# Kernel tuning notes

Hardware: AMD Instinct MI355X
Metric: run time of the kernel (lower is better)

## Reference

```python
import jax, jax.numpy as jnp
import numpy as np

B, N_TOK, C = 64, 256, 1024
H = 16
PH, PW = 16, 16  # patch (window) size; N_TOK == PH*PW
D_FF = 4 * C
EPS = 1e-5


def rel_pos_idx(ph, pw):
    # Swin-style relative position index for a ph x pw window -> [ph*pw * ph*pw]
    coords_h = np.arange(ph)
    coords_w = np.arange(pw)
    coords = np.stack(np.meshgrid(coords_h, coords_w, indexing='ij'))  # [2, ph, pw]
    coords = coords.reshape(2, -1)  # [2, N]
    rel = coords[:, :, None] - coords[:, None, :]  # [2, N, N]
    rel = rel.transpose(1, 2, 0)  # [N, N, 2]
    rel[:, :, 0] += ph - 1
    rel[:, :, 1] += pw - 1
    rel[:, :, 0] *= 2 * pw - 1
    return rel.sum(-1).reshape(-1).astype(np.int32)  # [N*N]


def layernorm(x, g, b):
    mu = jnp.mean(x, axis=-1, keepdims=True)
    var = jnp.mean(jnp.square(x - mu), axis=-1, keepdims=True)
    return (x - mu) * jax.lax.rsqrt(var + EPS) * g + b


def setup_inputs() -> dict:
    key = jax.random.key(0)
    ks = jax.random.split(key, 12)
    s = lambda fan: 1.0 / np.sqrt(fan)
    inp = {
        'x': jax.random.normal(ks[0], (B, N_TOK, C), dtype=jnp.float32),
        'rel_pos_idx': jnp.asarray(rel_pos_idx(PH, PW)),
        'qkv_w': jax.random.normal(ks[1], (C, 3 * C), dtype=jnp.float32) * s(C),
        'qkv_b': jnp.zeros((3 * C,), dtype=jnp.float32),
        'proj_w': jax.random.normal(ks[2], (C, C), dtype=jnp.float32) * s(C),
        'proj_b': jnp.zeros((C,), dtype=jnp.float32),
        'rel_pos_bias': jax.random.uniform(ks[3], ((2 * PH - 1) * (2 * PW - 1), H), dtype=jnp.float32),
        'ln1_g': jnp.ones((C,), dtype=jnp.float32),
        'ln1_b': jnp.zeros((C,), dtype=jnp.float32),
        'ln2_g': jnp.ones((C,), dtype=jnp.float32),
        'ln2_b': jnp.zeros((C,), dtype=jnp.float32),
        'fc1_w': jax.random.normal(ks[4], (C, D_FF), dtype=jnp.float32) * s(C),
        'fc1_b': jnp.zeros((D_FF,), dtype=jnp.float32),
        'fc2_w': jax.random.normal(ks[5], (D_FF, C), dtype=jnp.float32) * s(D_FF),
        'fc2_b': jnp.zeros((C,), dtype=jnp.float32),
    }
    return inp


def reference(x, rel_pos_idx, qkv_w, qkv_b, proj_w, proj_b, rel_pos_bias,
              ln1_g, ln1_b, ln2_g, ln2_b, fc1_w, fc1_b, fc2_w, fc2_b):
    Bc, N, Cc = x.shape
    Dh = Cc // H
    scale = Dh ** -0.5

    # --- token mixer: RelAttention with pre-norm residual ---
    h = layernorm(x, ln1_g, ln1_b)
    qkv = (h @ qkv_w + qkv_b).reshape(Bc, N, 3, H, Dh)
    qkv = jnp.transpose(qkv, (2, 0, 3, 1, 4))  # [3, B, H, N, Dh]
    q, k, v = qkv[0] * scale, qkv[1], qkv[2]

    attn = jnp.einsum('bhnd,bhmd->bhnm', q, k)  # [B, H, N, N]
    # gathered relative position bias: [N*N] -> [N, N, H] -> [H, N, N]
    bias = rel_pos_bias[rel_pos_idx].reshape(N, N, H)
    attn = attn + jnp.transpose(bias, (2, 0, 1))[None]
    attn = jax.nn.softmax(attn, axis=-1)

    out = jnp.einsum('bhnm,bhmd->bhnd', attn, v)  # [B, H, N, Dh]
    out = jnp.transpose(out, (0, 2, 1, 3)).reshape(Bc, N, Cc)  # MergeHeads
    x = x + (out @ proj_w + proj_b)

    # --- MLP with pre-norm residual ---
    h2 = layernorm(x, ln2_g, ln2_b)
    h2 = jax.nn.gelu(h2 @ fc1_w + fc1_b)
    x = x + (h2 @ fc2_w + fc2_b)
    return x
```

## Files before the change

kernel.cpp:

```cpp
#include <hip/hip_runtime.h>
#include <hip/hip_bf16.h>
#include <math.h>

typedef __hip_bfloat16 bf16;
typedef __attribute__((ext_vector_type(8))) __bf16 bf16x8;
typedef __attribute__((ext_vector_type(4))) float f32x4;
typedef __attribute__((ext_vector_type(4))) unsigned u32x4;

#define NB 64
#define NTOK 256
#define CDIM 1024
#define NH 16
#define DH 64
#define DFF 4096
#define MROWS (NB * NTOK)

__device__ __forceinline__ float gelu_f(float x) {
    float t = 1.5957691216057308f * (x + 0.044715f * x * x * x);
    return x / (1.0f + __expf(-t));
}

__device__ __forceinline__ void gload_lds16(const void* g, void* l) {
    __builtin_amdgcn_global_load_lds((const __attribute__((address_space(1))) void*)g,
                                     (__attribute__((address_space(3))) void*)l,
                                     16, 0, 0);
}

__global__ void transpose_f32_bf16(const float* __restrict__ in, bf16* __restrict__ out,
                                   int R, int Cc) {
    __shared__ bf16 tile[32][33];
    int c0 = blockIdx.x * 32, r0 = blockIdx.y * 32;
    int t = threadIdx.x;
    int r = t >> 5, c = t & 31;
#pragma unroll
    for (int i = 0; i < 4; i++)
        tile[r + i * 8][c] = (bf16)in[(size_t)(r0 + r + i * 8) * Cc + c0 + c];
    __syncthreads();
#pragma unroll
    for (int i = 0; i < 4; i++)
        out[(size_t)(c0 + r + i * 8) * R + r0 + c] = tile[c][r + i * 8];
}

__global__ __launch_bounds__(256) void ln_kernel(const float* __restrict__ xin,
                                                 const float* __restrict__ g,
                                                 const float* __restrict__ b,
                                                 bf16* __restrict__ outp) {
    __shared__ float red[8];
    int row = blockIdx.x, t = threadIdx.x;
    float4 v = ((const float4*)(xin + (size_t)row * CDIM))[t];
    float s = v.x + v.y + v.z + v.w;
    float q = v.x * v.x + v.y * v.y + v.z * v.z + v.w * v.w;
#pragma unroll
    for (int off = 32; off > 0; off >>= 1) {
        s += __shfl_down(s, off);
        q += __shfl_down(q, off);
    }
    int wave = t >> 6;
    if ((t & 63) == 0) { red[wave] = s; red[4 + wave] = q; }
    __syncthreads();
    float st = red[0] + red[1] + red[2] + red[3];
    float qt = red[4] + red[5] + red[6] + red[7];
    float mu = st * (1.0f / CDIM);
    float rstd = rsqrtf(qt * (1.0f / CDIM) - mu * mu + 1e-5f);
    float4 gv = ((const float4*)g)[t];
    float4 bv = ((const float4*)b)[t];
    bf16* orow = outp + (size_t)row * CDIM + t * 4;
    orow[0] = (bf16)((v.x - mu) * rstd * gv.x + bv.x);
    orow[1] = (bf16)((v.y - mu) * rstd * gv.y + bv.y);
    orow[2] = (bf16)((v.z - mu) * rstd * gv.z + bv.z);
    orow[3] = (bf16)((v.w - mu) * rstd * gv.w + bv.w);
}

__global__ void biasq_kernel(const int* __restrict__ idx, const float* __restrict__ rpb,
                             float* __restrict__ bq) {
    int e = blockIdx.x * 256 + threadIdx.x;
    int j = e & 3, lr = (e >> 2) & 15, ck = (e >> 6) & 3, q = (e >> 8) & 255, h = e >> 16;
    int k = ck * 64 + j * 16 + lr;
    bq[e] = rpb[idx[q * 256 + k] * NH + h];
}

__global__ __launch_bounds__(512, 2) void gemm_bt_kernel(
    const bf16* __restrict__ Abf, const bf16* __restrict__ Btbf,
    const float* __restrict__ bias, const float* resid,
    void* outp, size_t qstride, int M, int N, int K, int mode) {
    __shared__ __align__(16) u32x4 SL[4][2][1024];
    const unsigned short* A = (const unsigned short*)Abf;
    const unsigned short* Bt = (const unsigned short*)Btbf;
    int tid = threadIdx.x;
    int wave = tid >> 6, lane = tid & 63;
    int quad = lane >> 4, lr = lane & 15;
    int wm = (wave >> 2) << 7;
    int wn = (wave & 3) << 6;

    unsigned nx = gridDim.x;
    unsigned nwg = nx * gridDim.y;
    unsigned orig = blockIdx.y * nx + blockIdx.x;
    unsigned q8 = nwg >> 3, r8 = nwg & 7u;
    unsigned xcd = orig & 7u, io = orig >> 3;
    unsigned wg = (xcd < r8 ? xcd * (q8 + 1u) : r8 * (q8 + 1u) + (xcd - r8) * q8) + io;
    size_t row0 = (size_t)(wg / nx) << 8;
    size_t col0 = (size_t)(wg % nx) << 8;

    const unsigned short* Ag = A + row0 * K;
    const unsigned short* Bg = Bt + col0 * K;
    f32x4 acc[8][4] = {};

    const int wbase = tid & ~63;

    auto stage = [&](int s) {
        int slot = s & 3;
        int kbase = s << 5;
#pragma unroll
        for (int it = 0; it < 2; it++) {
            int ch = it * 512 + tid;
            int kk = ch >> 8, r = ch & 255;
            gload_lds16(Ag + (size_t)r * K + (kbase + kk * 8),
                        (void*)&SL[slot][0][it * 512 + wbase]);
        }
#pragma unroll
        for (int it = 0; it < 2; it++) {
            int ch = it * 512 + tid;
            int kk = ch >> 8, r = ch & 255;
            gload_lds16(Bg + (size_t)r * K + (kbase + kk * 8),
                        (void*)&SL[slot][1][it * 512 + wbase]);
        }
    };

    int S = K >> 5;
    stage(0);
    stage(1);
    for (int s = 0; s < S; s++) {
        if (s + 2 < S) {
            stage(s + 2);
            asm volatile("s_waitcnt vmcnt(8)" ::: "memory");
        } else if (s + 1 < S) {
            asm volatile("s_waitcnt vmcnt(4)" ::: "memory");
        } else {
            asm volatile("s_waitcnt vmcnt(0)" ::: "memory");
        }
        __builtin_amdgcn_s_barrier();
        asm volatile("" ::: "memory");

        int slot = s & 3;
        bf16x8 bfr[4];
#pragma unroll
        for (int j = 0; j < 4; j++)
            bfr[j] = __builtin_bit_cast(bf16x8, SL[slot][1][quad * 256 + wn + j * 16 + lr]);
#pragma unroll
        for (int ih = 0; ih < 2; ih++) {
            bf16x8 af[4];
#pragma unroll
            for (int i = 0; i < 4; i++)
                af[i] = __builtin_bit_cast(bf16x8,
                    SL[slot][0][quad * 256 + wm + (ih * 4 + i) * 16 + lr]);
            __builtin_amdgcn_s_setprio(1);
#pragma unroll
            for (int i = 0; i < 4; i++)
#pragma unroll
                for (int j = 0; j < 4; j++)
                    acc[ih * 4 + i][j] = __builtin_amdgcn_mfma_f32_16x16x32_bf16(
                        af[i], bfr[j], acc[ih * 4 + i][j], 0, 0, 0);
            __builtin_amdgcn_s_setprio(0);
        }
    }

    float bc[4];
#pragma unroll
    for (int j = 0; j < 4; j++) bc[j] = bias[col0 + wn + j * 16 + lr];
#pragma unroll
    for (int i = 0; i < 8; i++) {
#pragma unroll
        for (int r = 0; r < 4; r++) {
            int R = (int)row0 + wm + i * 16 + quad * 4 + r;
#pragma unroll
            for (int j = 0; j < 4; j++) {
                int Cc = (int)col0 + wn + j * 16 + lr;
                float val = acc[i][j][r] + bc[j];
                if (mode == 0) {
                    if (Cc < 1024) val *= 0.125f;
                    ((bf16*)outp)[(size_t)R * N + Cc] = (bf16)val;
                } else if (mode == 2) {
                    ((bf16*)outp)[(size_t)R * N + Cc] = (bf16)gelu_f(val);
                } else {
                    val += resid[(size_t)R * N + Cc];
                    ((float*)outp)[(size_t)R * N + Cc] = val;
                }
            }
        }
    }
}

__global__ __launch_bounds__(256, 2) void attn_mfma(
    const bf16* __restrict__ qkv, const float* __restrict__ biasq,
    bf16* __restrict__ outp, size_t qstride) {
    __shared__ u32x4 Ks4[1024];
    __shared__ unsigned Vt32[4096];
    __shared__ u32x4 PQ4[2048];

    int bh = blockIdx.x, lb = bh >> 4, h = bh & 15;
    int tid = threadIdx.x, wave = tid >> 6, lane = tid & 63;
    int quad = lane >> 4, lr = lane & 15;
    int wq = wave << 6;
    int tok0 = lb << 8;
    const unsigned short* base = (const unsigned short*)qkv;
    const unsigned short* qg = base + (size_t)tok0 * 3072 + h * DH;

    u32x4* pqw = PQ4 + wave * 512;
#pragma unroll
    for (int it = 0; it < 8; it++) {
        int c = it * 64 + lane;
        int qrow = c >> 3, p = c & 7;
        pqw[qrow * 8 + (p ^ (qrow & 7))] =
            *(const u32x4*)(qg + (size_t)(wq + qrow) * 3072 + p * 8);
    }
    bf16x8 qf[4][2];
#pragma unroll
    for (int i = 0; i < 4; i++)
#pragma unroll
        for (int ks = 0; ks < 2; ks++) {
            int qrow = i * 16 + lr;
            qf[i][ks] = __builtin_bit_cast(bf16x8,
                pqw[qrow * 8 + (((ks << 2) + quad) ^ (qrow & 7))]);
        }

    f32x4 o[4][4] = {};
    float mrun[4][4], lpart[4][4];
#pragma unroll
    for (int i = 0; i < 4; i++)
#pragma unroll
        for (int r = 0; r < 4; r++) { mrun[i][r] = -1e30f; lpart[i][r] = 0.f; }

    const float* bq = biasq + (size_t)h * 65536;

    for (int half = 0; half < 2; half++) {
        __syncthreads();
        const unsigned short* kg = base + (size_t)(tok0 + half * 128) * 3072 + CDIM + h * DH;
#pragma unroll
        for (int it = 0; it < 4; it++) {
            int c = it * 256 + tid;
            int kr = c >> 3, p = c & 7;
            Ks4[kr * 8 + (p ^ (kr & 7))] = *(const u32x4*)(kg + (size_t)kr * 3072 + p * 8);
        }
        const unsigned short* vg = base + (size_t)(tok0 + half * 128) * 3072 + 2 * CDIM + h * DH;
#pragma unroll
        for (int it = 0; it < 16; it++) {
            int idx = it * 256 + tid;
            int d = idx & 63, k2 = idx >> 6;
            unsigned lo = vg[(size_t)(2 * k2) * 3072 + d];
            unsigned hi = vg[(size_t)(2 * k2 + 1) * 3072 + d];
            int ck = k2 >> 2, w = k2 & 3;
            Vt32[d * 64 + ((ck ^ (d & 15)) << 2) + w] = lo | (hi << 16);
        }
        __syncthreads();

        for (int kb = 0; kb < 2; kb++) {
            f32x4 s[4][4] = {};
#pragma unroll
            for (int ks = 0; ks < 2; ks++) {
                bf16x8 kf[4];
#pragma unroll
                for (int j = 0; j < 4; j++) {
                    int kr = kb * 64 + j * 16 + lr;
                    kf[j] = __builtin_bit_cast(bf16x8,
                        Ks4[kr * 8 + (((ks << 2) + quad) ^ (kr & 7))]);
                }
#pragma unroll
                for (int i = 0; i < 4; i++)
#pragma unroll
                    for (int j = 0; j < 4; j++)
                        s[i][j] = __builtin_amdgcn_mfma_f32_16x16x32_bf16(
                            qf[i][ks], kf[j], s[i][j], 0, 0, 0);
            }
            int ckb = half * 2 + kb;
#pragma unroll
            for (int i = 0; i < 4; i++) {
#pragma unroll
                for (int r = 0; r < 4; r++) {
                    int q = wq + i * 16 + quad * 4 + r;
                    float4 bv = *(const float4*)(bq + (size_t)q * 256 + ckb * 64 + lr * 4);
                    float v0 = s[i][0][r] + bv.x;
                    float v1 = s[i][1][r] + bv.y;
                    float v2 = s[i][2][r] + bv.z;
                    float v3 = s[i][3][r] + bv.w;
                    float mx = fmaxf(fmaxf(v0, v1), fmaxf(v2, v3));
                    mx = fmaxf(mx, __shfl_xor(mx, 1));
                    mx = fmaxf(mx, __shfl_xor(mx, 2));
                    mx = fmaxf(mx, __shfl_xor(mx, 4));
                    mx = fmaxf(mx, __shfl_xor(mx, 8));
                    float mnew = fmaxf(mrun[i][r], mx);
                    float alpha = __expf(mrun[i][r] - mnew);
                    mrun[i][r] = mnew;
                    v0 = __expf(v0 - mnew);
                    v1 = __expf(v1 - mnew);
                    v2 = __expf(v2 - mnew);
                    v3 = __expf(v3 - mnew);
                    lpart[i][r] = lpart[i][r] * alpha + (v0 + v1 + v2 + v3);
                    s[i][0][r] = v0; s[i][1][r] = v1; s[i][2][r] = v2; s[i][3][r] = v3;
#pragma unroll
                    for (int dj = 0; dj < 4; dj++) o[i][dj][r] *= alpha;
                }
            }
            bf16* pqb = (bf16*)pqw;
#pragma unroll
            for (int i = 0; i < 4; i++)
#pragma unroll
                for (int r = 0; r < 4; r++) {
                    int ql = i * 16 + quad * 4 + r;
#pragma unroll
                    for (int j = 0; j < 4; j++) {
                        int col = j * 16 + lr;
                        int ck = col >> 3;
                        pqb[ql * 64 + ((ck ^ (ql & 7)) << 3) + (col & 7)] =
                            (bf16)s[i][j][r];
                    }
                }
            asm volatile("s_waitcnt lgkmcnt(0)" ::: "memory");
#pragma unroll
            for (int ks2 = 0; ks2 < 2; ks2++) {
                bf16x8 pf[4], vf[4];
#pragma unroll
                for (int i = 0; i < 4; i++) {
                    int ql = i * 16 + lr;
                    pf[i] = __builtin_bit_cast(bf16x8,
                        pqw[ql * 8 + (((ks2 << 2) + quad) ^ (ql & 7))]);
                }
#pragma unroll
                for (int dj = 0; dj < 4; dj++) {
                    int d = dj * 16 + lr;
                    int ck = kb * 8 + ks2 * 4 + quad;
                    vf[dj] = __builtin_bit_cast(bf16x8,
                        *(const u32x4*)(Vt32 + d * 64 + ((ck ^ (d & 15)) << 2)));
                }
#pragma unroll
                for (int i = 0; i < 4; i++)
#pragma unroll
                    for (int dj = 0; dj < 4; dj++)
                        o[i][dj] = __builtin_amdgcn_mfma_f32_16x16x32_bf16(
                            pf[i], vf[dj], o[i][dj], 0, 0, 0);
            }
        }
    }

    bf16* ob = (bf16*)pqw;
#pragma unroll
    for (int i = 0; i < 4; i++)
#pragma unroll
        for (int r = 0; r < 4; r++) {
            float lp = lpart[i][r];
            lp += __shfl_xor(lp, 1);
            lp += __shfl_xor(lp, 2);
            lp += __shfl_xor(lp, 4);
            lp += __shfl_xor(lp, 8);
            float inv = 1.0f / lp;
            int row = i * 16 + quad * 4 + r;
#pragma unroll
            for (int dj = 0; dj < 4; dj++) {
                int col = dj * 16 + lr;
                int ck = col >> 3;
                ob[row * 64 + ((ck ^ (row & 7)) << 3) + (col & 7)] =
                    (bf16)(o[i][dj][r] * inv);
            }
        }
    asm volatile("s_waitcnt lgkmcnt(0)" ::: "memory");
#pragma unroll
    for (int it = 0; it < 8; it++) {
        int c = it * 64 + lane;
        int row = c >> 3, p = c & 7;
        u32x4 v = pqw[row * 8 + (p ^ (row & 7))];
        *(u32x4*)(outp + (size_t)(tok0 + wq + row) * CDIM + h * DH + p * 8) = v;
    }
}

extern "C" void kernel_launch(void* const* d_in, const int* in_sizes, int n_in,
                              void* d_out, int out_size, void* d_ws, size_t ws_size,
                              hipStream_t stream) {
    const float* x      = (const float*)d_in[0];
    const int*   rpi    = (const int*)d_in[1];
    const float* qkv_w  = (const float*)d_in[2];
    const float* qkv_b  = (const float*)d_in[3];
    const float* proj_w = (const float*)d_in[4];
    const float* proj_b = (const float*)d_in[5];
    const float* rpb    = (const float*)d_in[6];
    const float* ln1g   = (const float*)d_in[7];
    const float* ln1b   = (const float*)d_in[8];
    const float* ln2g   = (const float*)d_in[9];
    const float* ln2b   = (const float*)d_in[10];
    const float* fc1_w  = (const float*)d_in[11];
    const float* fc1_b  = (const float*)d_in[12];
    const float* fc2_w  = (const float*)d_in[13];
    const float* fc2_b  = (const float*)d_in[14];
    float* out = (float*)d_out;
    char* ws = (char*)d_ws;

    bf16* qkvT   = (bf16*)(ws);
    bf16* projT  = (bf16*)(ws + 6291456ull);
    bf16* fc1T   = (bf16*)(ws + 8388608ull);
    bf16* fc2T   = (bf16*)(ws + 16777216ull);
    float* biasq = (float*)(ws + 25165824ull);
    const size_t fixed_end = 29360128ull;

    long long avail = (long long)ws_size - (long long)fixed_end;
    long long rc = avail / 10240;
    rc &= ~255LL;
    if (rc < 256) rc = 256;
    if (rc > MROWS) rc = MROWS;
    const int Rc = (int)rc;
    bf16* hbuf   = (bf16*)(ws + fixed_end);
    bf16* bigbuf = (bf16*)(ws + fixed_end + (size_t)Rc * 2048ull);

    transpose_f32_bf16<<<dim3(3072 / 32, 1024 / 32), 256, 0, stream>>>(qkv_w, qkvT, 1024, 3072);
    transpose_f32_bf16<<<dim3(1024 / 32, 1024 / 32), 256, 0, stream>>>(proj_w, projT, 1024, 1024);
    transpose_f32_bf16<<<dim3(4096 / 32, 1024 / 32), 256, 0, stream>>>(fc1_w, fc1T, 1024, 4096);
    transpose_f32_bf16<<<dim3(1024 / 32, 4096 / 32), 256, 0, stream>>>(fc2_w, fc2T, 4096, 1024);
    biasq_kernel<<<4096, 256, 0, stream>>>(rpi, rpb, biasq);

    for (int r0 = 0; r0 < MROWS; r0 += Rc) {
        int m = MROWS - r0 < Rc ? MROWS - r0 : Rc;
        ln_kernel<<<m, 256, 0, stream>>>(x + (size_t)r0 * CDIM, ln1g, ln1b, hbuf);
        gemm_bt_kernel<<<dim3(3072 / 256, m / 256), 512, 0, stream>>>(
            hbuf, qkvT, qkv_b, nullptr, bigbuf, 0, m, 3072, 1024, 0);
        attn_mfma<<<(m / 256) * NH, 256, 0, stream>>>(bigbuf, biasq, hbuf, 0);
        gemm_bt_kernel<<<dim3(1024 / 256, m / 256), 512, 0, stream>>>(
            hbuf, projT, proj_b, x + (size_t)r0 * CDIM, out + (size_t)r0 * CDIM, 0,
            m, 1024, 1024, 3);
    }

    for (int r0 = 0; r0 < MROWS; r0 += Rc) {
        int m = MROWS - r0 < Rc ? MROWS - r0 : Rc;
        ln_kernel<<<m, 256, 0, stream>>>(out + (size_t)r0 * CDIM, ln2g, ln2b, hbuf);
        gemm_bt_kernel<<<dim3(4096 / 256, m / 256), 512, 0, stream>>>(
            hbuf, fc1T, fc1_b, nullptr, bigbuf, 0, m, 4096, 1024, 2);
        gemm_bt_kernel<<<dim3(1024 / 256, m / 256), 512, 0, stream>>>(
            bigbuf, fc2T, fc2_b, out + (size_t)r0 * CDIM, out + (size_t)r0 * CDIM, 0,
            m, 1024, 4096, 3);
    }
}
```

Before: 1.219 ms.

## Shrink GEMM tile to 256x128 with double-buffered LDS and higher occupancy

The GEMM block tile narrows from 256x256 to 256x128, so each wave now computes a 64x64 sub-tile instead of 128x64. The LDS ring drops from four stages to two, with a second barrier before each refill, and launch bounds now ask for 4 blocks per CU. The goal is to cut registers and LDS per block so more blocks run at once, giving more latency hiding and more blocks per launch. In exchange, each loaded byte is reused less and the shallower prefetch plus the extra barrier can expose memory latency.

```diff
diff --git a/kernel.cpp b/kernel.cpp
--- a/kernel.cpp
+++ b/kernel.cpp
@@ -79,18 +79,19 @@
     bq[e] = rpb[idx[q * 256 + k] * NH + h];
 }
 
-__global__ __launch_bounds__(512, 2) void gemm_bt_kernel(
+__global__ __launch_bounds__(512, 4) void gemm_bt_kernel(
     const bf16* __restrict__ Abf, const bf16* __restrict__ Btbf,
     const float* __restrict__ bias, const float* resid,
     void* outp, size_t qstride, int M, int N, int K, int mode) {
-    __shared__ __align__(16) u32x4 SL[4][2][1024];
+    __shared__ __align__(16) u32x4 SA[2][1024];
+    __shared__ __align__(16) u32x4 SB[2][512];
     const unsigned short* A = (const unsigned short*)Abf;
     const unsigned short* Bt = (const unsigned short*)Btbf;
     int tid = threadIdx.x;
     int wave = tid >> 6, lane = tid & 63;
     int quad = lane >> 4, lr = lane & 15;
-    int wm = (wave >> 2) << 7;
-    int wn = (wave & 3) << 6;
+    int wm = (wave >> 1) << 6;
+    int wn = (wave & 1) << 6;
 
     unsigned nx = gridDim.x;
     unsigned nwg = nx * gridDim.y;
@@ -99,30 +100,28 @@
     unsigned xcd = orig & 7u, io = orig >> 3;
     unsigned wg = (xcd < r8 ? xcd * (q8 + 1u) : r8 * (q8 + 1u) + (xcd - r8) * q8) + io;
     size_t row0 = (size_t)(wg / nx) << 8;
-    size_t col0 = (size_t)(wg % nx) << 8;
+    size_t col0 = (size_t)(wg % nx) << 7;
 
     const unsigned short* Ag = A + row0 * K;
     const unsigned short* Bg = Bt + col0 * K;
-    f32x4 acc[8][4] = {};
+    f32x4 acc[4][4] = {};
 
     const int wbase = tid & ~63;
 
     auto stage = [&](int s) {
-        int slot = s & 3;
+        int slot = s & 1;
         int kbase = s << 5;
 #pragma unroll
         for (int it = 0; it < 2; it++) {
             int ch = it * 512 + tid;
             int kk = ch >> 8, r = ch & 255;
             gload_lds16(Ag + (size_t)r * K + (kbase + kk * 8),
-                        (void*)&SL[slot][0][it * 512 + wbase]);
-        }
-#pragma unroll
-        for (int it = 0; it < 2; it++) {
-            int ch = it * 512 + tid;
-            int kk = ch >> 8, r = ch & 255;
+                        (void*)&SA[slot][it * 512 + wbase]);
+        }
+        {
+            int kk = tid >> 7, r = tid & 127;
             gload_lds16(Bg + (size_t)r * K + (kbase + kk * 8),
-                        (void*)&SL[slot][1][it * 512 + wbase]);
+                        (void*)&SB[slot][wbase]);
         }
     };
 
@@ -130,45 +129,40 @@
     stage(0);
     stage(1);
     for (int s = 0; s < S; s++) {
-        if (s + 2 < S) {
-            stage(s + 2);
-            asm volatile("s_waitcnt vmcnt(8)" ::: "memory");
-        } else if (s + 1 < S) {
-            asm volatile("s_waitcnt vmcnt(4)" ::: "memory");
+        int slot = s & 1;
+        if (s + 1 < S) {
+            asm volatile("s_waitcnt vmcnt(3)" ::: "memory");
         } else {
             asm volatile("s_waitcnt vmcnt(0)" ::: "memory");
         }
         __builtin_amdgcn_s_barrier();
         asm volatile("" ::: "memory");
 
-        int slot = s & 3;
-        bf16x8 bfr[4];
+        bf16x8 bfr[4], af[4];
 #pragma unroll
         for (int j = 0; j < 4; j++)
-            bfr[j] = __builtin_bit_cast(bf16x8, SL[slot][1][quad * 256 + wn + j * 16 + lr]);
-#pragma unroll
-        for (int ih = 0; ih < 2; ih++) {
-            bf16x8 af[4];
-#pragma unroll
-            for (int i = 0; i < 4; i++)
-                af[i] = __builtin_bit_cast(bf16x8,
-                    SL[slot][0][quad * 256 + wm + (ih * 4 + i) * 16 + lr]);
-            __builtin_amdgcn_s_setprio(1);
-#pragma unroll
-            for (int i = 0; i < 4; i++)
-#pragma unroll
-                for (int j = 0; j < 4; j++)
-                    acc[ih * 4 + i][j] = __builtin_amdgcn_mfma_f32_16x16x32_bf16(
-                        af[i], bfr[j], acc[ih * 4 + i][j], 0, 0, 0);
-            __builtin_amdgcn_s_setprio(0);
-        }
+            bfr[j] = __builtin_bit_cast(bf16x8, SB[slot][quad * 128 + wn + j * 16 + lr]);
+#pragma unroll
+        for (int i = 0; i < 4; i++)
+            af[i] = __builtin_bit_cast(bf16x8, SA[slot][quad * 256 + wm + i * 16 + lr]);
+        __builtin_amdgcn_s_setprio(1);
+#pragma unroll
+        for (int i = 0; i < 4; i++)
+#pragma unroll
+            for (int j = 0; j < 4; j++)
+                acc[i][j] = __builtin_amdgcn_mfma_f32_16x16x32_bf16(af[i], bfr[j],
+                                                                    acc[i][j], 0, 0, 0);
+        __builtin_amdgcn_s_setprio(0);
+        asm volatile("" ::: "memory");
+        __builtin_amdgcn_s_barrier();
+        if (s + 2 < S) stage(s + 2);
     }
 
     float bc[4];
 #pragma unroll
     for (int j = 0; j < 4; j++) bc[j] = bias[col0 + wn + j * 16 + lr];
 #pragma unroll
-    for (int i = 0; i < 8; i++) {
+    for (int i = 0; i < 4; i++) {
 #pragma unroll
         for (int r = 0; r < 4; r++) {
             int R = (int)row0 + wm + i * 16 + quad * 4 + r;
@@ -417,10 +411,10 @@
     for (int r0 = 0; r0 < MROWS; r0 += Rc) {
         int m = MROWS - r0 < Rc ? MROWS - r0 : Rc;
         ln_kernel<<<m, 256, 0, stream>>>(x + (size_t)r0 * CDIM, ln1g, ln1b, hbuf);
-        gemm_bt_kernel<<<dim3(3072 / 256, m / 256), 512, 0, stream>>>(
+        gemm_bt_kernel<<<dim3(3072 / 128, m / 256), 512, 0, stream>>>(
             hbuf, qkvT, qkv_b, nullptr, bigbuf, 0, m, 3072, 1024, 0);
         attn_mfma<<<(m / 256) * NH, 256, 0, stream>>>(bigbuf, biasq, hbuf, 0);
-        gemm_bt_kernel<<<dim3(1024 / 256, m / 256), 512, 0, stream>>>(
+        gemm_bt_kernel<<<dim3(1024 / 128, m / 256), 512, 0, stream>>>(
             hbuf, projT, proj_b, x + (size_t)r0 * CDIM, out + (size_t)r0 * CDIM, 0,
             m, 1024, 1024, 3);
     }
@@ -428,9 +422,9 @@
     for (int r0 = 0; r0 < MROWS; r0 += Rc) {
         int m = MROWS - r0 < Rc ? MROWS - r0 : Rc;
         ln_kernel<<<m, 256, 0, stream>>>(out + (size_t)r0 * CDIM, ln2g, ln2b, hbuf);
-        gemm_bt_kernel<<<dim3(4096 / 256, m / 256), 512, 0, stream>>>(
+        gemm_bt_kernel<<<dim3(4096 / 128, m / 256), 512, 0, stream>>>(
             hbuf, fc1T, fc1_b, nullptr, bigbuf, 0, m, 4096, 1024, 2);
-        gemm_bt_kernel<<<dim3(1024 / 256, m / 256), 512, 0, stream>>>(
+        gemm_bt_kernel<<<dim3(1024 / 128, m / 256), 512, 0, stream>>>(
             bigbuf, fc2T, fc2_b, out + (size_t)r0 * CDIM, out + (size_t)r0 * CDIM, 0,
             m, 1024, 4096, 3);
     }
```

Measured after the change: 1.294 ms. +6.1%, slower.
